# Kernel optimization log

Measured on AMD Instinct MI355X. Metric: run time of the kernel, lower is better.

The kernel has to match this reference:

```python
import jax, jax.numpy as jnp
import numpy as np
import math

B, S, E, H, FF = 8, 1024, 1024, 16, 4096
HD = E // H
N_DOM = 1024          # boolean-domain size used in the custom scale
LN_EPS = 1e-5


def _layernorm(x, g, b, eps=LN_EPS):
    mu = jnp.mean(x, axis=-1, keepdims=True)
    var = jnp.var(x, axis=-1, keepdims=True)
    return (x - mu) * jax.lax.rsqrt(var + eps) * g + b


def setup_inputs() -> dict:
    key = jax.random.key(0)
    ks = jax.random.split(key, 8)
    s_e = 1.0 / math.sqrt(E)
    s_f = 1.0 / math.sqrt(FF)
    return {
        "x": jax.random.normal(ks[0], (B, S, E), jnp.float32),
        "in_proj_w": jax.random.normal(ks[1], (3 * E, E), jnp.float32) * s_e,
        "out_proj_w": jax.random.normal(ks[2], (E, E), jnp.float32) * s_e,
        "ln1_g": jnp.ones((E,), jnp.float32),
        "ln1_b": jnp.zeros((E,), jnp.float32),
        "ln2_g": jnp.ones((E,), jnp.float32),
        "ln2_b": jnp.zeros((E,), jnp.float32),
        "w1": jax.random.normal(ks[3], (FF, E), jnp.float32) * s_e,
        "b1": jax.random.normal(ks[4], (FF,), jnp.float32) * 0.01,
        "w2": jax.random.normal(ks[5], (E, FF), jnp.float32) * s_f,
        "b2": jax.random.normal(ks[6], (E,), jnp.float32) * 0.01,
    }


def reference(x, in_proj_w, out_proj_w, ln1_g, ln1_b, ln2_g, ln2_b, w1, b1, w2, b2):
    # --- custom multi-head attention (bias=False, dropout=0) ---
    qkv = jnp.einsum("bse,fe->bsf", x, in_proj_w)              # [B,S,3E]
    q, k, v = jnp.split(qkv, 3, axis=-1)
    q = q.reshape(B, S, H, HD)
    k = k.reshape(B, S, H, HD)
    v = v.reshape(B, S, H, HD)
    # nonstandard scale: sqrt(1/head_dim) * 2 * log(N)
    scale = math.sqrt(1.0 / HD) * 2.0 * math.log(N_DOM)
    scores = jnp.einsum("bqhd,bkhd->bhqk", q * scale, k)       # [B,H,S,S]
    attn = jax.nn.softmax(scores, axis=-1)
    ctx = jnp.einsum("bhqk,bkhd->bqhd", attn, v).reshape(B, S, E)
    attn_out = jnp.einsum("bse,fe->bsf", ctx, out_proj_w)      # [B,S,E]
    # --- residual + norm + FFN + residual + norm ---
    h = _layernorm(x + attn_out, ln1_g, ln1_b)
    ff = jnp.einsum("bsf,ef->bse", jax.nn.relu(jnp.einsum("bse,fe->bsf", h, w1) + b1), w2) + b2
    return _layernorm(h + ff, ln2_g, ln2_b)
```

## Files before the change

### kernel.cpp

```cpp
#include <hip/hip_runtime.h>
#include <cstdint>
#include <cmath>


typedef _Float16 f16;
typedef _Float16 f16x8 __attribute__((ext_vector_type(8)));
typedef _Float16 f16x4 __attribute__((ext_vector_type(4)));
typedef __bf16   bf16;
typedef __bf16   bf16x8 __attribute__((ext_vector_type(8)));
typedef __bf16   bf16x4 __attribute__((ext_vector_type(4)));
typedef float    f32x4  __attribute__((ext_vector_type(4)));

#define B_SZ  8
#define S_SZ  1024
#define E_SZ  1024
#define H_SZ  16
#define HD_SZ 64
#define FF_SZ 4096
#define MTOK  (B_SZ * S_SZ)

__device__ __forceinline__ void async_ld16(const void* g, void* l) {
  __builtin_amdgcn_global_load_lds(
      (const __attribute__((address_space(1))) void*)(uintptr_t)g,
      (__attribute__((address_space(3))) void*)(uint32_t)(uintptr_t)l,
      16, 0, 0);
}

__global__ void cast_kernel(const float* __restrict__ in, f16* __restrict__ out, int n4) {
  int i = blockIdx.x * blockDim.x + threadIdx.x;
  if (i < n4) {
    float4 f = ((const float4*)in)[i];
    f16x4 o = {(f16)f.x, (f16)f.y, (f16)f.z, (f16)f.w};
    ((f16x4*)out)[i] = o;
  }
}

template <bool OUT_F16, bool RELU>
__global__ void gemm_bt(const f16* __restrict__ A, const f16* __restrict__ Bm,
                        const float* __restrict__ bias, void* __restrict__ Cp,
                        int M, int N, int K, int bf16_from_bn) {
  __shared__ f16 As[128 * 64];
  __shared__ f16 Bs[128 * 64];

  const int tid  = threadIdx.x;
  const int wave = tid >> 6;
  const int lane = tid & 63;
  const int quad = lane >> 4;
  const int l16  = lane & 15;
  const int c7   = l16 & 7;
  const int wr   = wave >> 1;
  const int wc   = wave & 1;
  const int bm   = blockIdx.y;
  const int bn   = blockIdx.x;

  f32x4 acc[4][4];
#pragma unroll
  for (int i = 0; i < 4; i++)
#pragma unroll
    for (int j = 0; j < 4; j++) acc[i][j] = (f32x4){0.f, 0.f, 0.f, 0.f};

  const int rii  = wave * 8 + (lane >> 3);
  const int soct = (lane & 7) ^ (rii & 7);
  const f16* gA = A + ((size_t)bm * 128 + rii) * (size_t)K + soct * 8;
  const f16* gB = Bm + ((size_t)bn * 128 + rii) * (size_t)K + soct * 8;

  for (int k0 = 0; k0 < K; k0 += 64) {
    __syncthreads();
#pragma unroll
    for (int i = 0; i < 4; i++)
      async_ld16(gA + (size_t)i * 32 * K + k0, &As[(i * 32 + wave * 8) * 64]);
#pragma unroll
    for (int i = 0; i < 4; i++)
      async_ld16(gB + (size_t)i * 32 * K + k0, &Bs[(i * 32 + wave * 8) * 64]);
    __syncthreads();

#pragma unroll
    for (int kd2 = 0; kd2 < 2; kd2++) {
      f16x8 af[4], bfv[4];
#pragma unroll
      for (int mi = 0; mi < 4; mi++)
        af[mi] = *(const f16x8*)&As[(wr * 64 + mi * 16 + l16) * 64 + (((kd2 * 4 + quad) ^ c7) << 3)];
#pragma unroll
      for (int ni = 0; ni < 4; ni++)
        bfv[ni] = *(const f16x8*)&Bs[(wc * 64 + ni * 16 + l16) * 64 + (((kd2 * 4 + quad) ^ c7) << 3)];
#pragma unroll
      for (int mi = 0; mi < 4; mi++)
#pragma unroll
        for (int ni = 0; ni < 4; ni++)
          acc[mi][ni] = __builtin_amdgcn_mfma_f32_16x16x32_f16(af[mi], bfv[ni], acc[mi][ni], 0, 0, 0);
    }
  }

  const int rowBase = bm * 128 + wr * 64;
  const int colBase = bn * 128 + wc * 64;
  const bool store_bf16 = OUT_F16 && (bn >= bf16_from_bn);
#pragma unroll
  for (int ni = 0; ni < 4; ni++) {
    const int col = colBase + ni * 16 + l16;
    const float bv = (bias != nullptr) ? bias[col] : 0.f;
#pragma unroll
    for (int mi = 0; mi < 4; mi++) {
#pragma unroll
      for (int r = 0; r < 4; r++) {
        const int row = rowBase + mi * 16 + quad * 4 + r;
        float v = acc[mi][ni][r] + bv;
        if (RELU) v = fmaxf(v, 0.f);
        if (OUT_F16) {
          if (store_bf16)
            ((bf16*)Cp)[(size_t)row * N + col] = (bf16)v;
          else
            ((f16*)Cp)[(size_t)row * N + col] = (f16)v;
        } else {
          ((float*)Cp)[(size_t)row * N + col] = v;
        }
      }
    }
  }
}

__global__ __launch_bounds__(256, 3)
void attn_kernel(const f16* __restrict__ qkv, f16* __restrict__ ctx,
                 float scale2, float c2) {
  __shared__ __align__(16) char pool[49664];
  f16*  Qs = (f16*)pool;
  bf16* Ps = (bf16*)pool;
  bf16* Vt = (bf16*)(pool + 16384);
  f16*  Ks = (f16*)(pool + 33280);

  const int tid  = threadIdx.x;
  const int wave = tid >> 6;
  const int lane = tid & 63;
  const int quad = lane >> 4;
  const int l16  = lane & 15;
  const int c7   = l16 & 7;

  const int flat = blockIdx.x;
  const int bh   = flat & 127;
  const int qt   = flat >> 7;
  const int b    = bh >> 4;
  const int h    = bh & 15;

  const int rs = 3 * E_SZ;
  const size_t tokbase = (size_t)b * S_SZ;

  const int su  = lane >> 3;
  const int soc = (lane & 7) ^ su;

  {
    const f16* gq = qkv + (tokbase + qt * 128 + wave * 8 + su) * (size_t)rs + h * HD_SZ + soc * 8;
#pragma unroll
    for (int i = 0; i < 4; i++)
      async_ld16(gq + (size_t)i * 32 * rs, pool + (i * 32 + wave * 8) * 128);
  }
  __syncthreads();

  f16x8 aq[2][2];
#pragma unroll
  for (int mi = 0; mi < 2; mi++)
#pragma unroll
    for (int kd = 0; kd < 2; kd++) {
      const int row = wave * 32 + mi * 16 + l16;
      aq[mi][kd] = *(const f16x8*)&Qs[row * 64 + (((kd * 4 + quad) ^ c7) << 3)];
    }

  float Lpart[2] = {0.f, 0.f};
  f32x4 oacc[2][4];
#pragma unroll
  for (int mi = 0; mi < 2; mi++)
#pragma unroll
    for (int ni = 0; ni < 4; ni++) oacc[mi][ni] = (f32x4){0.f, 0.f, 0.f, 0.f};

  const int vc  = (tid & 7) * 8;
  const int vk0 = (tid >> 3) * 4;

  for (int t = 0; t < S_SZ / 128; t++) {
    __syncthreads();
    {
      const f16* gk = qkv + (tokbase + t * 128 + wave * 8 + su) * (size_t)rs + E_SZ + h * HD_SZ + soc * 8;
#pragma unroll
      for (int i = 0; i < 4; i++)
        async_ld16(gk + (size_t)i * 32 * rs, pool + 33280 + (i * 32 + wave * 8) * 128);
    }
    {
      const bf16* gv = (const bf16*)qkv + (tokbase + t * 128 + vk0) * (size_t)rs + 2 * E_SZ + h * HD_SZ + vc;
      bf16x8 v0 = *(const bf16x8*)(gv);
      bf16x8 v1 = *(const bf16x8*)(gv + rs);
      bf16x8 v2 = *(const bf16x8*)(gv + 2 * rs);
      bf16x8 v3 = *(const bf16x8*)(gv + 3 * rs);
#pragma unroll
      for (int e = 0; e < 8; e++) {
        bf16x4 pk = {v0[e], v1[e], v2[e], v3[e]};
        *(bf16x4*)&Vt[(vc + e) * 132 + vk0] = pk;
      }
    }
    __syncthreads();

    f32x4 sacc[2][8];
#pragma unroll
    for (int mi = 0; mi < 2; mi++)
#pragma unroll
      for (int nt = 0; nt < 8; nt++) sacc[mi][nt] = (f32x4){0.f, 0.f, 0.f, 0.f};
#pragma unroll
    for (int nt = 0; nt < 8; nt++) {
      const int krow = nt * 16 + l16;
#pragma unroll
      for (int kd = 0; kd < 2; kd++) {
        f16x8 bk = *(const f16x8*)&Ks[krow * 64 + (((kd * 4 + quad) ^ c7) << 3)];
#pragma unroll
        for (int mi = 0; mi < 2; mi++)
          sacc[mi][nt] = __builtin_amdgcn_mfma_f32_16x16x32_f16(bk, aq[mi][kd], sacc[mi][nt], 0, 0, 0);
      }
    }

#pragma unroll
    for (int mi = 0; mi < 2; mi++) {
#pragma unroll
      for (int nt = 0; nt < 8; nt++) {
#pragma unroll
        for (int r = 0; r < 4; r++) {
          float p = exp2f(fmaf(sacc[mi][nt][r], scale2, -c2));
          sacc[mi][nt][r] = p;
          Lpart[mi] += p;
        }
      }
    }

#pragma unroll
    for (int hf = 0; hf < 2; hf++) {
#pragma unroll
      for (int mi = 0; mi < 2; mi++) {
        const int prow = wave * 32 + mi * 16 + l16;
#pragma unroll
        for (int ntl = 0; ntl < 4; ntl++) {
          const f32x4 s4 = sacc[mi][hf * 4 + ntl];
          bf16x4 pk = {(bf16)s4[0], (bf16)s4[1], (bf16)s4[2], (bf16)s4[3]};
          const int oct = (2 * ntl + (quad >> 1)) ^ c7;
          *(bf16x4*)&Ps[prow * 64 + oct * 8 + (quad & 1) * 4] = pk;
        }
      }
#pragma unroll
      for (int kt = 0; kt < 2; kt++) {
        bf16x8 ap[2];
#pragma unroll
        for (int mi = 0; mi < 2; mi++) {
          const int prow = wave * 32 + mi * 16 + l16;
          ap[mi] = *(const bf16x8*)&Ps[prow * 64 + (((kt * 4 + quad) ^ c7) << 3)];
        }
#pragma unroll
        for (int ni = 0; ni < 4; ni++) {
          const int d = ni * 16 + l16;
          bf16x4 blo = *(const bf16x4*)&Vt[d * 132 + hf * 64 + kt * 32 + quad * 8];
          bf16x4 bhi = *(const bf16x4*)&Vt[d * 132 + hf * 64 + kt * 32 + quad * 8 + 4];
          bf16x8 bv = __builtin_shufflevector(blo, bhi, 0, 1, 2, 3, 4, 5, 6, 7);
#pragma unroll
          for (int mi = 0; mi < 2; mi++)
            oacc[mi][ni] = __builtin_amdgcn_mfma_f32_16x16x32_bf16(ap[mi], bv, oacc[mi][ni], 0, 0, 0);
        }
      }
    }
  }

#pragma unroll
  for (int mi = 0; mi < 2; mi++) {
    float Lfull = Lpart[mi];
    Lfull += __shfl_xor(Lfull, 16, 64);
    Lfull += __shfl_xor(Lfull, 32, 64);
#pragma unroll
    for (int r = 0; r < 4; r++) {
      const float Lr  = __shfl(Lfull, quad * 4 + r, 64);
      const float inv = 1.f / Lr;
      const int s = qt * 128 + wave * 32 + mi * 16 + quad * 4 + r;
#pragma unroll
      for (int ni = 0; ni < 4; ni++)
        ctx[(tokbase + s) * (size_t)E_SZ + h * HD_SZ + ni * 16 + l16] = (f16)(oacc[mi][ni][r] * inv);
    }
  }
}

__global__ void ln_kernel(const float* __restrict__ a, const float* __restrict__ res,
                          const float* __restrict__ g, const float* __restrict__ bta,
                          float* __restrict__ out32, f16* __restrict__ out16) {
  const int row  = blockIdx.x;
  const int tid  = threadIdx.x;
  const int wave = tid >> 6;
  const int lane = tid & 63;
  const size_t base = (size_t)row * 1024;
  const int c = tid * 4;

  float4 va = *(const float4*)&a[base + c];
  float4 vr = *(const float4*)&res[base + c];
  float v0 = va.x + vr.x, v1 = va.y + vr.y, v2 = va.z + vr.z, v3 = va.w + vr.w;

  __shared__ float r1[4], r2[4];
  float s = v0 + v1 + v2 + v3;
#pragma unroll
  for (int off = 32; off; off >>= 1) s += __shfl_xor(s, off, 64);
  if (lane == 0) r1[wave] = s;
  __syncthreads();
  const float mu = (r1[0] + r1[1] + r1[2] + r1[3]) * (1.f / 1024.f);

  float d0 = v0 - mu, d1 = v1 - mu, d2 = v2 - mu, d3 = v3 - mu;
  float ss = d0 * d0 + d1 * d1 + d2 * d2 + d3 * d3;
#pragma unroll
  for (int off = 32; off; off >>= 1) ss += __shfl_xor(ss, off, 64);
  if (lane == 0) r2[wave] = ss;
  __syncthreads();
  const float var = (r2[0] + r2[1] + r2[2] + r2[3]) * (1.f / 1024.f);
  const float rsq = rsqrtf(var + 1e-5f);

  float4 gg = *(const float4*)&g[c];
  float4 bb = *(const float4*)&bta[c];
  float o0 = d0 * rsq * gg.x + bb.x;
  float o1 = d1 * rsq * gg.y + bb.y;
  float o2 = d2 * rsq * gg.z + bb.z;
  float o3 = d3 * rsq * gg.w + bb.w;
  float4 o = {o0, o1, o2, o3};
  *(float4*)&out32[base + c] = o;
  if (out16 != nullptr) {
    f16x4 ob = {(f16)o0, (f16)o1, (f16)o2, (f16)o3};
    *(f16x4*)&out16[base + c] = ob;
  }
}

extern "C" void kernel_launch(void* const* d_in, const int* in_sizes, int n_in,
                              void* d_out, int out_size, void* d_ws, size_t ws_size,
                              hipStream_t stream) {
  const float* x    = (const float*)d_in[0];
  const float* wqkv = (const float*)d_in[1];
  const float* wo   = (const float*)d_in[2];
  const float* ln1g = (const float*)d_in[3];
  const float* ln1b = (const float*)d_in[4];
  const float* ln2g = (const float*)d_in[5];
  const float* ln2b = (const float*)d_in[6];
  const float* w1   = (const float*)d_in[7];
  const float* b1   = (const float*)d_in[8];
  const float* w2   = (const float*)d_in[9];
  const float* b2   = (const float*)d_in[10];
  float* out = (float*)d_out;

  char* ws = (char*)d_ws;
  f16* w_inb  = (f16*)(ws + 0);
  f16* w_outb = (f16*)(ws + 6291456);
  f16* w1b    = (f16*)(ws + 8388608);
  f16* w2b    = (f16*)(ws + 16777216);
  f16* xb     = (f16*)(ws + 25165824);
  f16* qkv    = (f16*)(ws + 41943040);
  f16* ctx    = (f16*)(ws + 92274688);
  f16* ff1    = (f16*)(ws + 41943040);
  float* tmp  = (float*)(ws + 109051904);
  float* hbuf = (float*)(ws + 142606336);
  f16* hb     = xb;

  const int NOBF = 1 << 30;

  cast_kernel<<<3072, 256, 0, stream>>>(wqkv, w_inb, 3 * E_SZ * E_SZ / 4);
  cast_kernel<<<1024, 256, 0, stream>>>(wo, w_outb, E_SZ * E_SZ / 4);
  cast_kernel<<<4096, 256, 0, stream>>>(w1, w1b, FF_SZ * E_SZ / 4);
  cast_kernel<<<4096, 256, 0, stream>>>(w2, w2b, E_SZ * FF_SZ / 4);
  cast_kernel<<<8192, 256, 0, stream>>>(x, xb, MTOK * E_SZ / 4);

  gemm_bt<true, false><<<dim3(3 * E_SZ / 128, MTOK / 128), 256, 0, stream>>>(
      xb, w_inb, nullptr, qkv, MTOK, 3 * E_SZ, E_SZ, 16);

  attn_kernel<<<1024, 256, 0, stream>>>(qkv, ctx, 2.5f, 60.0f);

  gemm_bt<false, false><<<dim3(E_SZ / 128, MTOK / 128), 256, 0, stream>>>(
      ctx, w_outb, nullptr, tmp, MTOK, E_SZ, E_SZ, NOBF);

  ln_kernel<<<MTOK, 256, 0, stream>>>(tmp, x, ln1g, ln1b, hbuf, hb);

  gemm_bt<true, true><<<dim3(FF_SZ / 128, MTOK / 128), 256, 0, stream>>>(
      hb, w1b, b1, ff1, MTOK, FF_SZ, E_SZ, NOBF);

  gemm_bt<false, false><<<dim3(E_SZ / 128, MTOK / 128), 256, 0, stream>>>(
      ff1, w2b, b2, tmp, MTOK, E_SZ, FF_SZ, NOBF);

  ln_kernel<<<MTOK, 256, 0, stream>>>(tmp, hbuf, ln2g, ln2b, out, nullptr);

  (void)in_sizes; (void)n_in; (void)out_size; (void)ws_size;
}
```

Before: 504.7 us.

## Rework attention to 32x32 MFMA with in-register P via permlane swaps

The attention kernel switches from 16x16x32 to 32x32x16 MFMA tiles. It keeps the softmax probabilities in registers, using permlane32_swap to reshape the score accumulator into the A-operand layout for the PV matmul, so the LDS round-trip for P goes away. LDS use drops because the Q/P region is removed and K reuses the Q buffer after Q is loaded into registers. That allows occupancy to rise from 3 to 4 blocks per CU, and s_setprio hints are added around the MFMA sections. The risks are a lane-permutation or row-mapping error in the new accumulator layout and higher register pressure under the tighter launch bounds.

New measurement: 493.4 us. 2.2% less time.

```diff
diff --git a/kernel.cpp b/kernel.cpp
--- a/kernel.cpp
+++ b/kernel.cpp
@@ -9,7 +9,11 @@
 typedef __bf16   bf16;
 typedef __bf16   bf16x8 __attribute__((ext_vector_type(8)));
 typedef __bf16   bf16x4 __attribute__((ext_vector_type(4)));
+typedef __bf16   bf16x2 __attribute__((ext_vector_type(2)));
 typedef float    f32x4  __attribute__((ext_vector_type(4)));
+typedef float    f32x16 __attribute__((ext_vector_type(16)));
+typedef unsigned int uint2v __attribute__((ext_vector_type(2)));
+typedef unsigned int u32x4v __attribute__((ext_vector_type(4)));
 
 #define B_SZ  8
 #define S_SZ  1024
@@ -24,6 +28,12 @@
       (const __attribute__((address_space(1))) void*)(uintptr_t)g,
       (__attribute__((address_space(3))) void*)(uint32_t)(uintptr_t)l,
       16, 0, 0);
+}
+
+__device__ __forceinline__ void permswap(uint32_t& a, uint32_t& b) {
+  uint2v r = __builtin_amdgcn_permlane32_swap(a, b, false, false);
+  a = r[0];
+  b = r[1];
 }
 
 __global__ void cast_kernel(const float* __restrict__ in, f16* __restrict__ out, int n4) {
@@ -118,21 +128,18 @@
   }
 }
 
-__global__ __launch_bounds__(256, 3)
+__global__ __launch_bounds__(256, 4)
 void attn_kernel(const f16* __restrict__ qkv, f16* __restrict__ ctx,
                  float scale2, float c2) {
-  __shared__ __align__(16) char pool[49664];
-  f16*  Qs = (f16*)pool;
-  bf16* Ps = (bf16*)pool;
+  __shared__ __align__(16) char pool[33280];
+  f16*  Ks = (f16*)pool;
   bf16* Vt = (bf16*)(pool + 16384);
-  f16*  Ks = (f16*)(pool + 33280);
 
   const int tid  = threadIdx.x;
   const int wave = tid >> 6;
   const int lane = tid & 63;
-  const int quad = lane >> 4;
-  const int l16  = lane & 15;
-  const int c7   = l16 & 7;
+  const int l31  = lane & 31;
+  const int hi   = lane >> 5;
 
   const int flat = blockIdx.x;
   const int bh   = flat & 127;
@@ -154,21 +161,20 @@
   }
   __syncthreads();
 
-  f16x8 aq[2][2];
-#pragma unroll
-  for (int mi = 0; mi < 2; mi++)
-#pragma unroll
-    for (int kd = 0; kd < 2; kd++) {
-      const int row = wave * 32 + mi * 16 + l16;
-      aq[mi][kd] = *(const f16x8*)&Qs[row * 64 + (((kd * 4 + quad) ^ c7) << 3)];
-    }
-
-  float Lpart[2] = {0.f, 0.f};
-  f32x4 oacc[2][4];
-#pragma unroll
-  for (int mi = 0; mi < 2; mi++)
-#pragma unroll
-    for (int ni = 0; ni < 4; ni++) oacc[mi][ni] = (f32x4){0.f, 0.f, 0.f, 0.f};
+  f16x8 aq[4];
+  {
+    const int qrow = wave * 32 + l31;
+#pragma unroll
+    for (int ks = 0; ks < 4; ks++)
+      aq[ks] = *(const f16x8*)&Ks[qrow * 64 + (((ks * 2 + hi) ^ (qrow & 7)) << 3)];
+  }
+
+  float Lp = 0.f;
+  f32x16 oacc[2];
+#pragma unroll
+  for (int nb = 0; nb < 2; nb++)
+#pragma unroll
+    for (int i = 0; i < 16; i++) oacc[nb][i] = 0.f;
 
   const int vc  = (tid & 7) * 8;
   const int vk0 = (tid >> 3) * 4;
@@ -179,7 +185,7 @@
       const f16* gk = qkv + (tokbase + t * 128 + wave * 8 + su) * (size_t)rs + E_SZ + h * HD_SZ + soc * 8;
 #pragma unroll
       for (int i = 0; i < 4; i++)
-        async_ld16(gk + (size_t)i * 32 * rs, pool + 33280 + (i * 32 + wave * 8) * 128);
+        async_ld16(gk + (size_t)i * 32 * rs, pool + (i * 32 + wave * 8) * 128);
     }
     {
       const bf16* gv = (const bf16*)qkv + (tokbase + t * 128 + vk0) * (size_t)rs + 2 * E_SZ + h * HD_SZ + vc;
@@ -195,85 +201,65 @@
     }
     __syncthreads();
 
-    f32x4 sacc[2][8];
-#pragma unroll
-    for (int mi = 0; mi < 2; mi++)
-#pragma unroll
-      for (int nt = 0; nt < 8; nt++) sacc[mi][nt] = (f32x4){0.f, 0.f, 0.f, 0.f};
-#pragma unroll
-    for (int nt = 0; nt < 8; nt++) {
-      const int krow = nt * 16 + l16;
-#pragma unroll
-      for (int kd = 0; kd < 2; kd++) {
-        f16x8 bk = *(const f16x8*)&Ks[krow * 64 + (((kd * 4 + quad) ^ c7) << 3)];
-#pragma unroll
-        for (int mi = 0; mi < 2; mi++)
-          sacc[mi][nt] = __builtin_amdgcn_mfma_f32_16x16x32_f16(bk, aq[mi][kd], sacc[mi][nt], 0, 0, 0);
-      }
-    }
-
-#pragma unroll
-    for (int mi = 0; mi < 2; mi++) {
-#pragma unroll
-      for (int nt = 0; nt < 8; nt++) {
-#pragma unroll
-        for (int r = 0; r < 4; r++) {
-          float p = exp2f(fmaf(sacc[mi][nt][r], scale2, -c2));
-          sacc[mi][nt][r] = p;
-          Lpart[mi] += p;
+#pragma unroll
+    for (int nt = 0; nt < 4; nt++) {
+      f32x16 sacc;
+#pragma unroll
+      for (int i = 0; i < 16; i++) sacc[i] = 0.f;
+
+      const int krow = nt * 32 + l31;
+      __builtin_amdgcn_s_setprio(1);
+#pragma unroll
+      for (int ks = 0; ks < 4; ks++) {
+        f16x8 kf = *(const f16x8*)&Ks[krow * 64 + (((ks * 2 + hi) ^ (krow & 7)) << 3)];
+        sacc = __builtin_amdgcn_mfma_f32_32x32x16_f16(kf, aq[ks], sacc, 0, 0, 0);
+      }
+      __builtin_amdgcn_s_setprio(0);
+
+      uint32_t w[8];
+#pragma unroll
+      for (int j = 0; j < 8; j++) {
+        float p0 = exp2f(fmaf(sacc[2 * j],     scale2, -c2));
+        float p1 = exp2f(fmaf(sacc[2 * j + 1], scale2, -c2));
+        Lp += p0 + p1;
+        bf16x2 pk2 = {(bf16)p0, (bf16)p1};
+        w[j] = __builtin_bit_cast(uint32_t, pk2);
+      }
+      permswap(w[0], w[2]);
+      permswap(w[1], w[3]);
+      permswap(w[4], w[6]);
+      permswap(w[5], w[7]);
+      u32x4v pe = {w[0], w[1], w[2], w[3]};
+      u32x4v po = {w[4], w[5], w[6], w[7]};
+      bf16x8 pa[2] = {__builtin_bit_cast(bf16x8, pe), __builtin_bit_cast(bf16x8, po)};
+
+      __builtin_amdgcn_s_setprio(1);
+#pragma unroll
+      for (int nb = 0; nb < 2; nb++) {
+        const int d = nb * 32 + l31;
+#pragma unroll
+        for (int kst = 0; kst < 2; kst++) {
+          const int key = (nt * 2 + kst) * 16 + hi * 8;
+          bf16x4 blo = *(const bf16x4*)&Vt[d * 132 + key];
+          bf16x4 bhi = *(const bf16x4*)&Vt[d * 132 + key + 4];
+          bf16x8 bv = __builtin_shufflevector(blo, bhi, 0, 1, 2, 3, 4, 5, 6, 7);
+          oacc[nb] = __builtin_amdgcn_mfma_f32_32x32x16_bf16(pa[kst], bv, oacc[nb], 0, 0, 0);
         }
       }
-    }
-
-#pragma unroll
-    for (int hf = 0; hf < 2; hf++) {
-#pragma unroll
-      for (int mi = 0; mi < 2; mi++) {
-        const int prow = wave * 32 + mi * 16 + l16;
-#pragma unroll
-        for (int ntl = 0; ntl < 4; ntl++) {
-          const f32x4 s4 = sacc[mi][hf * 4 + ntl];
-          bf16x4 pk = {(bf16)s4[0], (bf16)s4[1], (bf16)s4[2], (bf16)s4[3]};
-          const int oct = (2 * ntl + (quad >> 1)) ^ c7;
-          *(bf16x4*)&Ps[prow * 64 + oct * 8 + (quad & 1) * 4] = pk;
-        }
-      }
-#pragma unroll
-      for (int kt = 0; kt < 2; kt++) {
-        bf16x8 ap[2];
-#pragma unroll
-        for (int mi = 0; mi < 2; mi++) {
-          const int prow = wave * 32 + mi * 16 + l16;
-          ap[mi] = *(const bf16x8*)&Ps[prow * 64 + (((kt * 4 + quad) ^ c7) << 3)];
-        }
-#pragma unroll
-        for (int ni = 0; ni < 4; ni++) {
-          const int d = ni * 16 + l16;
-          bf16x4 blo = *(const bf16x4*)&Vt[d * 132 + hf * 64 + kt * 32 + quad * 8];
-          bf16x4 bhi = *(const bf16x4*)&Vt[d * 132 + hf * 64 + kt * 32 + quad * 8 + 4];
-          bf16x8 bv = __builtin_shufflevector(blo, bhi, 0, 1, 2, 3, 4, 5, 6, 7);
-#pragma unroll
-          for (int mi = 0; mi < 2; mi++)
-            oacc[mi][ni] = __builtin_amdgcn_mfma_f32_16x16x32_bf16(ap[mi], bv, oacc[mi][ni], 0, 0, 0);
-        }
-      }
-    }
-  }
-
-#pragma unroll
-  for (int mi = 0; mi < 2; mi++) {
-    float Lfull = Lpart[mi];
-    Lfull += __shfl_xor(Lfull, 16, 64);
-    Lfull += __shfl_xor(Lfull, 32, 64);
-#pragma unroll
-    for (int r = 0; r < 4; r++) {
-      const float Lr  = __shfl(Lfull, quad * 4 + r, 64);
-      const float inv = 1.f / Lr;
-      const int s = qt * 128 + wave * 32 + mi * 16 + quad * 4 + r;
-#pragma unroll
-      for (int ni = 0; ni < 4; ni++)
-        ctx[(tokbase + s) * (size_t)E_SZ + h * HD_SZ + ni * 16 + l16] = (f16)(oacc[mi][ni][r] * inv);
-    }
+      __builtin_amdgcn_s_setprio(0);
+    }
+  }
+
+  float Lfull = Lp + __shfl_xor(Lp, 32, 64);
+  const float inv = 1.f / Lfull;
+#pragma unroll
+  for (int r = 0; r < 16; r++) {
+    const int qrow = (r & 3) + 8 * (r >> 2) + 4 * hi;
+    const float invr = __shfl(inv, qrow, 32);
+    const size_t row = tokbase + (size_t)qt * 128 + wave * 32 + qrow;
+#pragma unroll
+    for (int nb = 0; nb < 2; nb++)
+      ctx[row * (size_t)E_SZ + h * HD_SZ + nb * 32 + l31] = (f16)(oacc[nb][r] * invr);
   }
 }
 
```
